# Optimization experiments

Measured on AMD Instinct MI355X. Metric: run time of the kernel, lower is better.

## Reference

```python
import jax, jax.numpy as jnp
import numpy as np
from jax import lax


def unfold(x, k, p, s):
    # torch.nn.functional.unfold: (N,C,H,W) -> (N, C*k*k, L)
    pat = lax.conv_general_dilated_patches(
        x, filter_shape=(k, k), window_strides=(s, s),
        padding=((p, p), (p, p)))
    n, ck2, ho, wo = pat.shape
    return pat.reshape(n, ck2, ho * wo)


def fold(cols, x_shape, k, p, s):
    # torch.nn.functional.fold == adjoint of unfold (overlap-add col2im)
    zero = jnp.zeros(x_shape, cols.dtype)
    _, vjp_fn = jax.vjp(lambda x: unfold(x, k, p, s), zero)
    return vjp_fn(cols)[0]


def setup_inputs() -> dict:
    key = jax.random.key(0)
    ks = jax.random.split(key, 5)
    N, C, H, W = 2, 256, 64, 64
    return {
        "lq_up": jax.random.normal(ks[0], (N, C, H, W), jnp.float32),
        "ref_downup": jax.random.normal(ks[1], (N, C, H, W), jnp.float32),
        "ref0": jax.random.normal(ks[2], (N, C, H, W), jnp.float32),
        "ref1": jax.random.normal(ks[3], (N, C // 2, 2 * H, 2 * W), jnp.float32),
        "ref2": jax.random.normal(ks[4], (N, C // 4, 4 * H, 4 * W), jnp.float32),
    }


def reference(lq_up, ref_downup, ref0, ref1, ref2):
    refs = (ref0, ref1, ref2)
    levels = len(refs)
    n, _, h, w = lq_up.shape

    query = unfold(lq_up, 3, 1, 1)          # (N, C*9, HW)
    key = unfold(ref_downup, 3, 1, 1)       # (N, C*9, HW)
    key_t = jnp.transpose(key, (0, 2, 1))   # (N, HW, C*9)

    eps = 1e-12
    key_t = key_t / jnp.maximum(
        jnp.linalg.norm(key_t, axis=2, keepdims=True), eps)
    query = query / jnp.maximum(
        jnp.linalg.norm(query, axis=1, keepdims=True), eps)

    rel = jnp.matmul(key_t, query)          # (N, HW_k, HW_q)
    max_val = jnp.max(rel, axis=1)          # (N, HW_q)
    max_index = jnp.argmax(rel, axis=1)     # (N, HW_q)

    textures = []
    for i in range(levels):
        k_i, p_i, s_i = 3 * 2 ** i, 2 ** i, 2 ** i
        v = unfold(refs[i], k_i, p_i, s_i)                     # (N, Ci*k*k, HW)
        t = jnp.take_along_axis(v, max_index[:, None, :], axis=2)
        t = fold(t, refs[i].shape, k_i, p_i, s_i) / 9.0
        textures.append(t)

    soft_attention = max_val.reshape(n, 1, h, w)
    return (soft_attention, textures[0], textures[1], textures[2])
```

## Files before the change

### kernel.cpp

```cpp
#include <hip/hip_runtime.h>
#include <math.h>

struct __attribute__((packed)) f4u { float v[4]; };

typedef __attribute__((ext_vector_type(8))) short bf16x8;
typedef __attribute__((ext_vector_type(4))) float f32x4;

#define KCH 16
#define NCH 256
#define LDF 40

__global__ __launch_bounds__(256) void sumsq_k(const float* __restrict__ lq,
                                               const float* __restrict__ refdu,
                                               float* __restrict__ S) {
  const float* src = blockIdx.z ? refdu : lq;
  const int n = blockIdx.y;
  const int h = blockIdx.x * 4 + (threadIdx.x >> 6);
  const int w = threadIdx.x & 63;
  const float* p = src + (size_t)n * 1048576 + h * 64 + w;
  float s0 = 0.f, s1 = 0.f, s2 = 0.f, s3 = 0.f;
  #pragma unroll 4
  for (int c = 0; c < 256; c += 4) {
    float x0 = p[(size_t)c * 4096];
    float x1 = p[(size_t)(c + 1) * 4096];
    float x2 = p[(size_t)(c + 2) * 4096];
    float x3 = p[(size_t)(c + 3) * 4096];
    s0 = fmaf(x0, x0, s0); s1 = fmaf(x1, x1, s1);
    s2 = fmaf(x2, x2, s2); s3 = fmaf(x3, x3, s3);
  }
  S[(blockIdx.z * 2 + n) * 4096 + h * 64 + w] = (s0 + s1) + (s2 + s3);
}

__global__ __launch_bounds__(256) void norm_k(const float* __restrict__ S,
                                              float* __restrict__ qinv,
                                              float* __restrict__ kinv) {
  int idx = blockIdx.x * 256 + threadIdx.x;
  int pix = idx & 4095;
  int nn  = (idx >> 12) & 1;
  int arr = idx >> 13;
  int ph = pix >> 6, pw = pix & 63;
  const float* Sp = S + (arr * 2 + nn) * 4096;
  float sum = 0.f;
  #pragma unroll
  for (int dy = -1; dy <= 1; ++dy) {
    int hh = ph + dy;
    if ((unsigned)hh < 64u) {
      const float* r = Sp + hh * 64;
      #pragma unroll
      for (int dx = -1; dx <= 1; ++dx) {
        int ww = pw + dx;
        if ((unsigned)ww < 64u) sum += r[ww];
      }
    }
  }
  float inv = 1.0f / fmaxf(sqrtf(sum), 1e-12f);
  if (arr) kinv[nn * 4096 + pix] = inv;
  else     qinv[nn * 4096 + pix] = inv;
}

__global__ __launch_bounds__(256) void conv_hl(const float* __restrict__ src,
                                               unsigned short* __restrict__ hi,
                                               unsigned short* __restrict__ lo) {
  int i = (blockIdx.x * 256 + threadIdx.x) * 4;
  float4 v = *reinterpret_cast<const float4*>(src + i);
  ushort4 h, l;
  float xs[4] = {v.x, v.y, v.z, v.w};
  unsigned short hs[4], ls[4];
  #pragma unroll
  for (int j = 0; j < 4; ++j) {
    float x = xs[j];
    unsigned u = __float_as_uint(x);
    unsigned hb = (u + 0x7FFFu + ((u >> 16) & 1u)) & 0xFFFF0000u;
    hs[j] = (unsigned short)(hb >> 16);
    float r = x - __uint_as_float(hb);
    unsigned ur = __float_as_uint(r);
    ls[j] = (unsigned short)((ur + 0x7FFFu + ((ur >> 16) & 1u)) >> 16);
  }
  h = make_ushort4(hs[0], hs[1], hs[2], hs[3]);
  l = make_ushort4(ls[0], ls[1], ls[2], ls[3]);
  *reinterpret_cast<ushort4*>(hi + i) = h;
  *reinterpret_cast<ushort4*>(lo + i) = l;
}

__global__ __launch_bounds__(256) void gemm_mfma(const unsigned short* __restrict__ Ah,
                                                 const unsigned short* __restrict__ Al,
                                                 const unsigned short* __restrict__ Bh,
                                                 const unsigned short* __restrict__ Bl,
                                                 float* __restrict__ Dbase,
                                                 int ldD, int C0, long long dstride) {
  __shared__ unsigned short LAh[64 * LDF], LAl[64 * LDF];
  __shared__ unsigned short LBh[64 * LDF], LBl[64 * LDF];
  const int tid = threadIdx.x;
  const int nz = blockIdx.z;
  const int k0 = blockIdx.x * 64;
  const int dcol0 = blockIdx.y * 64;
  const int jq0 = C0 + dcol0;
  float* D = Dbase + (size_t)nz * dstride;

  const bool oob = (jq0 < 0) || (jq0 + 64 > 4096);

  if (!oob) {
    const unsigned short* Ahb = Ah + (size_t)nz * 1048576;
    const unsigned short* Alb = Al + (size_t)nz * 1048576;
    const unsigned short* Bhb = Bh + (size_t)nz * 1048576;
    const unsigned short* Blb = Bl + (size_t)nz * 1048576;

    const int sh = tid & 1;
    const int mp = (tid >> 1) & 31;
    const int g  = tid >> 6;
    const int rowb = 8 * g + 4 * sh;
    const int colA = k0 + 2 * mp;
    const int colB = jq0 + 2 * mp;
    const int sIdx = (2 * mp) * LDF + g * 8 + sh * 4;

    const int wv = tid >> 6;
    const int lane = tid & 63;
    const int lm = lane & 15;
    const int lg = lane >> 4;
    const int offA = (wv * 16 + lm) * LDF + lg * 8;

    f32x4 acc[4];
    #pragma unroll
    for (int t = 0; t < 4; ++t) acc[t] = (f32x4){0.f, 0.f, 0.f, 0.f};

    for (int ct = 0; ct < 256; ct += 32) {
      __syncthreads();
      {
        const size_t r0 = (size_t)(ct + rowb) * 4096;
        unsigned a0 = *reinterpret_cast<const unsigned*>(Ahb + r0 + colA);
        unsigned a1 = *reinterpret_cast<const unsigned*>(Ahb + r0 + 4096 + colA);
        unsigned a2 = *reinterpret_cast<const unsigned*>(Ahb + r0 + 8192 + colA);
        unsigned a3 = *reinterpret_cast<const unsigned*>(Ahb + r0 + 12288 + colA);
        *reinterpret_cast<ushort4*>(&LAh[sIdx]) =
            make_ushort4(a0 & 0xffff, a1 & 0xffff, a2 & 0xffff, a3 & 0xffff);
        *reinterpret_cast<ushort4*>(&LAh[sIdx + LDF]) =
            make_ushort4(a0 >> 16, a1 >> 16, a2 >> 16, a3 >> 16);
        unsigned c0 = *reinterpret_cast<const unsigned*>(Alb + r0 + colA);
        unsigned c1 = *reinterpret_cast<const unsigned*>(Alb + r0 + 4096 + colA);
        unsigned c2 = *reinterpret_cast<const unsigned*>(Alb + r0 + 8192 + colA);
        unsigned c3 = *reinterpret_cast<const unsigned*>(Alb + r0 + 12288 + colA);
        *reinterpret_cast<ushort4*>(&LAl[sIdx]) =
            make_ushort4(c0 & 0xffff, c1 & 0xffff, c2 & 0xffff, c3 & 0xffff);
        *reinterpret_cast<ushort4*>(&LAl[sIdx + LDF]) =
            make_ushort4(c0 >> 16, c1 >> 16, c2 >> 16, c3 >> 16);
        unsigned b0 = *reinterpret_cast<const unsigned*>(Bhb + r0 + colB);
        unsigned b1 = *reinterpret_cast<const unsigned*>(Bhb + r0 + 4096 + colB);
        unsigned b2 = *reinterpret_cast<const unsigned*>(Bhb + r0 + 8192 + colB);
        unsigned b3 = *reinterpret_cast<const unsigned*>(Bhb + r0 + 12288 + colB);
        *reinterpret_cast<ushort4*>(&LBh[sIdx]) =
            make_ushort4(b0 & 0xffff, b1 & 0xffff, b2 & 0xffff, b3 & 0xffff);
        *reinterpret_cast<ushort4*>(&LBh[sIdx + LDF]) =
            make_ushort4(b0 >> 16, b1 >> 16, b2 >> 16, b3 >> 16);
        unsigned d0 = *reinterpret_cast<const unsigned*>(Blb + r0 + colB);
        unsigned d1 = *reinterpret_cast<const unsigned*>(Blb + r0 + 4096 + colB);
        unsigned d2 = *reinterpret_cast<const unsigned*>(Blb + r0 + 8192 + colB);
        unsigned d3 = *reinterpret_cast<const unsigned*>(Blb + r0 + 12288 + colB);
        *reinterpret_cast<ushort4*>(&LBl[sIdx]) =
            make_ushort4(d0 & 0xffff, d1 & 0xffff, d2 & 0xffff, d3 & 0xffff);
        *reinterpret_cast<ushort4*>(&LBl[sIdx + LDF]) =
            make_ushort4(d0 >> 16, d1 >> 16, d2 >> 16, d3 >> 16);
      }
      __syncthreads();
      bf16x8 a_h = *reinterpret_cast<const bf16x8*>(&LAh[offA]);
      bf16x8 a_l = *reinterpret_cast<const bf16x8*>(&LAl[offA]);
      #pragma unroll
      for (int t = 0; t < 4; ++t) {
        const int offB = (t * 16 + lm) * LDF + lg * 8;
        bf16x8 b_h = *reinterpret_cast<const bf16x8*>(&LBh[offB]);
        bf16x8 b_l = *reinterpret_cast<const bf16x8*>(&LBl[offB]);
        acc[t] = __builtin_amdgcn_mfma_f32_16x16x32_bf16(a_h, b_h, acc[t], 0, 0, 0);
        acc[t] = __builtin_amdgcn_mfma_f32_16x16x32_bf16(a_h, b_l, acc[t], 0, 0, 0);
        acc[t] = __builtin_amdgcn_mfma_f32_16x16x32_bf16(a_l, b_h, acc[t], 0, 0, 0);
      }
    }
    #pragma unroll
    for (int t = 0; t < 4; ++t) {
      #pragma unroll
      for (int r = 0; r < 4; ++r) {
        D[(size_t)(k0 + wv * 16 + lg * 4 + r) * ldD + dcol0 + t * 16 + lm] = acc[t][r];
      }
    }
  } else {
    const int row = tid & 63;
    const int cs = (tid >> 6) * 16;
    float* Dp = D + (size_t)(k0 + row) * ldD + dcol0 + cs;
    #pragma unroll
    for (int j = 0; j < 4; ++j)
      *reinterpret_cast<float4*>(Dp + j * 4) = make_float4(0.f, 0.f, 0.f, 0.f);
  }
}

__global__ __launch_bounds__(256) void reduce_max8(const float* __restrict__ Dbase,
                                                   int ldD, int C0, int Q0,
                                                   const float* __restrict__ kinv,
                                                   float* __restrict__ chunkv,
                                                   int* __restrict__ chunki,
                                                   int n0, long long dstride) {
  __shared__ float sk[KCH];
  const int n = n0 + blockIdx.z;
  const float* D = Dbase + (size_t)blockIdx.z * (size_t)dstride;
  const int k0 = blockIdx.y * KCH;
  const int kh = k0 >> 6;
  const int kwb = k0 & 63;
  if (threadIdx.x < KCH) sk[threadIdx.x] = kinv[n * 4096 + k0 + threadIdx.x];
  __syncthreads();
  const int q0 = Q0 + (blockIdx.x * 256 + threadIdx.x) * 8;
  const int qh = q0 >> 6;
  const int qw0 = q0 & 63;
  const bool up = (kh > 0) && (qh > 0);
  const bool dn = (kh < 63) && (qh < 63);
  const bool lf_ok = qw0 > 0;
  const bool rt_ok = qw0 < 56;
  float best[8]; int bidx[8];
  #pragma unroll
  for (int i = 0; i < 8; ++i) { best[i] = -INFINITY; bidx[i] = k0; }
  const float* Dq = D + (q0 - C0);
  const int step = ldD + 1;
  #pragma unroll 2
  for (int kk = 0; kk < KCH; ++kk) {
    const int kw = kwb + kk;
    const float* P = Dq + (size_t)(k0 + kk) * ldD;
    float r[8];
    {
      float4 c0 = *reinterpret_cast<const float4*>(P);
      float4 c1 = *reinterpret_cast<const float4*>(P + 4);
      r[0]=c0.x; r[1]=c0.y; r[2]=c0.z; r[3]=c0.w; r[4]=c1.x; r[5]=c1.y; r[6]=c1.z; r[7]=c1.w;
    }
    if (up) {
      float4 c0 = *reinterpret_cast<const float4*>(P - 64 * step);
      float4 c1 = *reinterpret_cast<const float4*>(P - 64 * step + 4);
      r[0]+=c0.x; r[1]+=c0.y; r[2]+=c0.z; r[3]+=c0.w; r[4]+=c1.x; r[5]+=c1.y; r[6]+=c1.z; r[7]+=c1.w;
    }
    if (dn) {
      float4 c0 = *reinterpret_cast<const float4*>(P + 64 * step);
      float4 c1 = *reinterpret_cast<const float4*>(P + 64 * step + 4);
      r[0]+=c0.x; r[1]+=c0.y; r[2]+=c0.z; r[3]+=c0.w; r[4]+=c1.x; r[5]+=c1.y; r[6]+=c1.z; r[7]+=c1.w;
    }
    if (kw > 0) {
      #pragma unroll
      for (int t = 0; t < 3; ++t) {
        if (t == 1 && !up) continue;
        if (t == 2 && !dn) continue;
        const int off = (t == 0) ? -step : (t == 1 ? -65 * step : 63 * step);
        f4u b0 = *reinterpret_cast<const f4u*>(P + off);
        f4u b1 = *reinterpret_cast<const f4u*>(P + off + 4);
        r[0] += lf_ok ? b0.v[0] : 0.f; r[1]+=b0.v[1]; r[2]+=b0.v[2]; r[3]+=b0.v[3];
        r[4]+=b1.v[0]; r[5]+=b1.v[1]; r[6]+=b1.v[2]; r[7]+=b1.v[3];
      }
    }
    if (kw < 63) {
      #pragma unroll
      for (int t = 0; t < 3; ++t) {
        if (t == 1 && !up) continue;
        if (t == 2 && !dn) continue;
        const int off = (t == 0) ? step : (t == 1 ? -63 * step : 65 * step);
        f4u b0 = *reinterpret_cast<const f4u*>(P + off);
        f4u b1 = *reinterpret_cast<const f4u*>(P + off + 4);
        r[0]+=b0.v[0]; r[1]+=b0.v[1]; r[2]+=b0.v[2]; r[3]+=b0.v[3];
        r[4]+=b1.v[0]; r[5]+=b1.v[1]; r[6]+=b1.v[2]; r[7] += rt_ok ? b1.v[3] : 0.f;
      }
    }
    const float s = sk[kk];
    const int k = k0 + kk;
    #pragma unroll
    for (int i = 0; i < 8; ++i) {
      float v = r[i] * s;
      if (v > best[i]) { best[i] = v; bidx[i] = k; }
    }
  }
  const int ob = (n * NCH + blockIdx.y) * 4096 + q0;
  *reinterpret_cast<float4*>(chunkv + ob)     = make_float4(best[0], best[1], best[2], best[3]);
  *reinterpret_cast<float4*>(chunkv + ob + 4) = make_float4(best[4], best[5], best[6], best[7]);
  *reinterpret_cast<int4*>(chunki + ob)     = make_int4(bidx[0], bidx[1], bidx[2], bidx[3]);
  *reinterpret_cast<int4*>(chunki + ob + 4) = make_int4(bidx[4], bidx[5], bidx[6], bidx[7]);
}

__global__ __launch_bounds__(256) void combine_k(const float* __restrict__ chunkv,
                                                 const int* __restrict__ chunki,
                                                 const float* __restrict__ qinv,
                                                 float* __restrict__ out_sa,
                                                 int* __restrict__ maxidx, int nch) {
  int t = blockIdx.x * 256 + threadIdx.x;
  int n = t >> 12, q = t & 4095;
  float best = -INFINITY;
  int bi = 0;
  for (int ch = 0; ch < nch; ++ch) {
    int ii = (n * nch + ch) * 4096 + q;
    float v = chunkv[ii];
    int ix = chunki[ii];
    if (v > best) { best = v; bi = ix; }
  }
  maxidx[t] = bi;
  out_sa[t] = best * qinv[t];
}

__global__ __launch_bounds__(256) void gemm_d(const float* __restrict__ Abase,
                                              const float* __restrict__ Bbase,
                                              float* __restrict__ Dbase,
                                              int ldD, int C0, long long dstride) {
  __shared__ __align__(16) float As[2][8][128];
  __shared__ __align__(16) float Bs[2][8][128];
  const int tid = threadIdx.x;
  const int nz = blockIdx.z;
  const int k0 = blockIdx.x * 128;
  const int j0 = blockIdx.y * 128;
  const float* A = Abase + (size_t)nz * 1048576;
  const float* B = Bbase + (size_t)nz * 1048576;
  float* D = Dbase + (size_t)nz * dstride;
  const int ty = tid >> 4, tx = tid & 15, lr = tid >> 5, lc = (tid & 31) << 2;
  float acc[8][8];
  #pragma unroll
  for (int i = 0; i < 8; ++i)
    #pragma unroll
    for (int j = 0; j < 8; ++j) acc[i][j] = 0.f;
  const bool oob = (C0 + j0 < 0) || (C0 + j0 + 128 > 4096);
  if (!oob) {
    const float* Ap = A + k0 + lc;
    const float* Bp = B + (C0 + j0) + lc;
    float4 av = *reinterpret_cast<const float4*>(Ap + (size_t)lr * 4096);
    float4 bv = *reinterpret_cast<const float4*>(Bp + (size_t)lr * 4096);
    *reinterpret_cast<float4*>(&As[0][lr][lc]) = av;
    *reinterpret_cast<float4*>(&Bs[0][lr][lc]) = bv;
    for (int ct = 0; ct < 256; ct += 8) {
      const int buf = (ct >> 3) & 1;
      __syncthreads();
      if (ct + 8 < 256) {
        av = *reinterpret_cast<const float4*>(Ap + (size_t)(ct + 8 + lr) * 4096);
        bv = *reinterpret_cast<const float4*>(Bp + (size_t)(ct + 8 + lr) * 4096);
      }
      #pragma unroll
      for (int kc = 0; kc < 8; ++kc) {
        float a[8], b[8];
        *reinterpret_cast<float4*>(&a[0]) = *reinterpret_cast<const float4*>(&As[buf][kc][ty * 4]);
        *reinterpret_cast<float4*>(&a[4]) = *reinterpret_cast<const float4*>(&As[buf][kc][64 + ty * 4]);
        *reinterpret_cast<float4*>(&b[0]) = *reinterpret_cast<const float4*>(&Bs[buf][kc][tx * 4]);
        *reinterpret_cast<float4*>(&b[4]) = *reinterpret_cast<const float4*>(&Bs[buf][kc][64 + tx * 4]);
        #pragma unroll
        for (int i = 0; i < 8; ++i)
          #pragma unroll
          for (int j = 0; j < 8; ++j)
            acc[i][j] = fmaf(a[i], b[j], acc[i][j]);
      }
      if (ct + 8 < 256) {
        *reinterpret_cast<float4*>(&As[buf ^ 1][lr][lc]) = av;
        *reinterpret_cast<float4*>(&Bs[buf ^ 1][lr][lc]) = bv;
      }
    }
  }
  #pragma unroll
  for (int half = 0; half < 2; ++half)
    #pragma unroll
    for (int i = 0; i < 4; ++i) {
      float* Dp = D + (size_t)(k0 + half * 64 + ty * 4 + i) * ldD + j0;
      *reinterpret_cast<float4*>(Dp + tx * 4)      = *reinterpret_cast<const float4*>(&acc[half * 4 + i][0]);
      *reinterpret_cast<float4*>(Dp + 64 + tx * 4) = *reinterpret_cast<const float4*>(&acc[half * 4 + i][4]);
    }
}

__global__ __launch_bounds__(256) void tex0_lds(const float* __restrict__ ref,
                                                const int* __restrict__ maxidx,
                                                float* __restrict__ outp) {
  __shared__ __align__(16) float4 L[4096];
  const int cq = blockIdx.x;
  const int n  = blockIdx.y;
  const int half = blockIdx.z;
  const int tid = threadIdx.x;
  const float* p0 = ref + (((size_t)n * 256 + cq * 4) << 12);
  for (int i = 0; i < 16; ++i) {
    int px = i * 256 + tid;
    L[px] = make_float4(p0[px], p0[px + 4096], p0[px + 8192], p0[px + 12288]);
  }
  __syncthreads();
  const int* mi = maxidx + n * 4096;
  float* ob = outp + (((size_t)n * 256 + cq * 4) << 12);
  for (int i = 0; i < 8; ++i) {
    int px = half * 2048 + i * 256 + tid;
    int y = px >> 6, x = px & 63;
    float ax = 0.f, ay = 0.f, az = 0.f, aw = 0.f;
    #pragma unroll
    for (int a = -1; a <= 1; ++a) {
      int jh = y + a;
      if ((unsigned)jh < 64u) {
        #pragma unroll
        for (int b = -1; b <= 1; ++b) {
          int jw = x + b;
          if ((unsigned)jw < 64u) {
            int m = mi[jh * 64 + jw];
            int rh = (m >> 6) - a;
            int cx = (m & 63) - b;
            if ((unsigned)rh < 64u && (unsigned)cx < 64u) {
              float4 v = L[rh * 64 + cx];
              ax += v.x; ay += v.y; az += v.z; aw += v.w;
            }
          }
        }
      }
    }
    ob[px]         = ax * (1.f / 9.f);
    ob[px + 4096]  = ay * (1.f / 9.f);
    ob[px + 8192]  = az * (1.f / 9.f);
    ob[px + 12288] = aw * (1.f / 9.f);
  }
}

__global__ __launch_bounds__(256) void tex1_lds(const float* __restrict__ ref,
                                                const int* __restrict__ maxidx,
                                                float* __restrict__ outp) {
  __shared__ __align__(16) float Lf[16384];
  const int c = blockIdx.x;
  const int n = blockIdx.y;
  const int half = blockIdx.z;
  const int tid = threadIdx.x;
  const float* p0 = ref + (((size_t)n * 128 + c) << 14);
  float4* L4 = (float4*)Lf;
  const float4* g4 = (const float4*)p0;
  for (int i = 0; i < 16; ++i) {
    int g = i * 256 + tid;
    L4[g] = g4[g];
  }
  __syncthreads();
  const int* mi = maxidx + n * 4096;
  float* ob = outp + (((size_t)n * 128 + c) << 14);
  for (int i = 0; i < 16; ++i) {
    int pp = half * 4096 + i * 256 + tid;
    int xp = pp & 63;
    int y  = pp >> 6;
    int jh0 = y >> 1;
    float a0 = 0.f, a1 = 0.f;
    #pragma unroll
    for (int a = -1; a <= 1; ++a) {
      int jh = jh0 + a;
      if ((unsigned)jh < 64u) {
        #pragma unroll
        for (int b = -1; b <= 1; ++b) {
          int jw = xp + b;
          if ((unsigned)jw < 64u) {
            int m = mi[jh * 64 + jw];
            int rh = (m >> 6) - a;
            int cx = (m & 63) - b;
            if ((unsigned)rh < 64u && (unsigned)cx < 64u) {
              int off = ((rh << 1) + (y & 1)) * 128 + (cx << 1);
              float2 v = *reinterpret_cast<const float2*>(&Lf[off]);
              a0 += v.x; a1 += v.y;
            }
          }
        }
      }
    }
    *reinterpret_cast<float2*>(&ob[y * 128 + xp * 2]) =
        make_float2(a0 * (1.f / 9.f), a1 * (1.f / 9.f));
  }
}

__global__ __launch_bounds__(256) void tex2_k(const float* __restrict__ ref,
                                              const int* __restrict__ maxidx,
                                              float* __restrict__ outp) {
  int gid = blockIdx.x * 256 + threadIdx.x;
  const int xg = gid & 63;
  const int y  = (gid >> 6) & 255;
  const int cc = (gid >> 14) & 7;
  const int n  = gid >> 17;
  const int jh0 = y >> 2;
  const int* mi = maxidx + n * 4096;
  int offs[9];
  #pragma unroll
  for (int a = -1; a <= 1; ++a) {
    #pragma unroll
    for (int b = -1; b <= 1; ++b) {
      const int t = (a + 1) * 3 + (b + 1);
      int jh = jh0 + a, jw = xg + b;
      int off = -1;
      if ((unsigned)jh < 64u && (unsigned)jw < 64u) {
        int m = mi[jh * 64 + jw];
        int rh = (m >> 6) - jh + jh0;
        int cx = (m & 63) - jw + xg;
        if ((unsigned)rh < 64u && (unsigned)cx < 64u)
          off = ((rh << 2) + (y & 3)) * 256 + (cx << 2);
      }
      offs[t] = off;
    }
  }
  const float* rb = ref + (((size_t)n * 64 + cc * 8) << 16);
  float* ob = outp + ((((size_t)n * 64 + cc * 8) * 256 + y) << 8) + xg * 4;
  #pragma unroll
  for (int i = 0; i < 8; ++i) {
    const float* r = rb + ((size_t)i << 16);
    float4 acc = make_float4(0.f, 0.f, 0.f, 0.f);
    #pragma unroll
    for (int t = 0; t < 9; ++t) {
      if (offs[t] >= 0) {
        float4 v = *reinterpret_cast<const float4*>(r + offs[t]);
        acc.x += v.x; acc.y += v.y; acc.z += v.z; acc.w += v.w;
      }
    }
    acc.x *= (1.f / 9.f); acc.y *= (1.f / 9.f); acc.z *= (1.f / 9.f); acc.w *= (1.f / 9.f);
    *reinterpret_cast<float4*>(ob + ((size_t)i << 16)) = acc;
  }
}

extern "C" void kernel_launch(void* const* d_in, const int* in_sizes, int n_in,
                              void* d_out, int out_size, void* d_ws, size_t ws_size,
                              hipStream_t stream) {
  const float* lq    = (const float*)d_in[0];
  const float* refdu = (const float*)d_in[1];
  const float* ref0  = (const float*)d_in[2];
  const float* ref1  = (const float*)d_in[3];
  const float* ref2  = (const float*)d_in[4];
  float* out = (float*)d_out;

  float* S      = (float*)d_ws;
  float* qinv   = S + 16384;
  float* kinv   = qinv + 8192;
  int*   maxidx = (int*)(kinv + 8192);
  float* chunkv = (float*)(maxidx + 8192);
  int*   chunki = (int*)(chunkv + 2097152);
  unsigned short* Ah = (unsigned short*)(chunki + 2097152);
  unsigned short* Al = Ah + 2097152;
  unsigned short* Bh = Al + 2097152;
  unsigned short* Bl = Bh + 2097152;
  const size_t aux_bytes = (size_t)(40960 + 2097152 + 2097152) * 4 + (size_t)4 * 2097152 * 2;
  float* D = (float*)((char*)d_ws + ((aux_bytes + 255) & ~(size_t)255));

  const int ldD = 4352;
  const size_t Dsz = (size_t)4096 * ldD * 4;
  const long long dstr = (long long)4096 * ldD;
  size_t avail = (ws_size > aux_bytes + 256) ? (ws_size - aux_bytes - 256) : 0;

  sumsq_k<<<dim3(16, 2, 2), 256, 0, stream>>>(lq, refdu, S);
  norm_k<<<dim3(64), 256, 0, stream>>>(S, qinv, kinv);

  if (avail >= 2 * Dsz) {
    conv_hl<<<dim3(2048), 256, 0, stream>>>(refdu, Ah, Al);
    conv_hl<<<dim3(2048), 256, 0, stream>>>(lq, Bh, Bl);
    gemm_mfma<<<dim3(64, 68, 2), 256, 0, stream>>>(Ah, Al, Bh, Bl, D, ldD, -128, dstr);
    reduce_max8<<<dim3(2, NCH, 2), 256, 0, stream>>>(D, ldD, -128, 0, kinv,
                                                     chunkv, chunki, 0, dstr);
  } else if (avail >= Dsz) {
    conv_hl<<<dim3(2048), 256, 0, stream>>>(refdu, Ah, Al);
    conv_hl<<<dim3(2048), 256, 0, stream>>>(lq, Bh, Bl);
    for (int n = 0; n < 2; ++n) {
      gemm_mfma<<<dim3(64, 68, 1), 256, 0, stream>>>(
          Ah + (size_t)n * 1048576, Al + (size_t)n * 1048576,
          Bh + (size_t)n * 1048576, Bl + (size_t)n * 1048576, D, ldD, -128, 0);
      reduce_max8<<<dim3(2, NCH, 1), 256, 0, stream>>>(D, ldD, -128, 0, kinv,
                                                       chunkv, chunki, n, 0);
    }
  } else {
    const int Wq = 2048, ldS = Wq + 256;
    for (int n = 0; n < 2; ++n) {
      for (int Q0 = 0; Q0 < 4096; Q0 += Wq) {
        int C0 = Q0 - 128;
        gemm_d<<<dim3(32, ldS / 128, 1), 256, 0, stream>>>(
            refdu + (size_t)n * 1048576, lq + (size_t)n * 1048576, D, ldS, C0, 0);
        reduce_max8<<<dim3(Wq / 2048, NCH, 1), 256, 0, stream>>>(
            D, ldS, C0, Q0, kinv, chunkv, chunki, n, 0);
      }
    }
  }
  combine_k<<<dim3(32), 256, 0, stream>>>(chunkv, chunki, qinv, out, maxidx, NCH);

  tex0_lds<<<dim3(64, 2, 2),  256, 0, stream>>>(ref0, maxidx, out + 8192);
  tex1_lds<<<dim3(128, 2, 2), 256, 0, stream>>>(ref1, maxidx, out + 2105344);
  tex2_k<<<dim3(1024), 256, 0, stream>>>(ref2, maxidx, out + 6299648);
}
```

Baseline: 434.4 us.

## Transpose bf16 split operands to pixel-major layout for vectorized GEMM tile loads

The hi/lo bf16 conversion kernel now transposes each input from channel-major to pixel-major order, going through a shared-memory tile. This lets the MFMA GEMM load its A and B tiles as contiguous 16-byte vectors per row instead of gathering 4-byte pairs across four channel rows and repacking them. The aim is to cut global load instruction count and the unpacking ALU work in the GEMM inner loop, at the cost of a more complex conversion kernel with LDS transposes and strided shared-memory reads.

```diff
diff --git a/kernel.cpp b/kernel.cpp
--- a/kernel.cpp
+++ b/kernel.cpp
@@ -58,38 +58,56 @@
   else     qinv[nn * 4096 + pix] = inv;
 }
 
-__global__ __launch_bounds__(256) void conv_hl(const float* __restrict__ src,
-                                               unsigned short* __restrict__ hi,
-                                               unsigned short* __restrict__ lo) {
-  int i = (blockIdx.x * 256 + threadIdx.x) * 4;
-  float4 v = *reinterpret_cast<const float4*>(src + i);
-  ushort4 h, l;
-  float xs[4] = {v.x, v.y, v.z, v.w};
-  unsigned short hs[4], ls[4];
+__global__ __launch_bounds__(256) void conv_t(const float* __restrict__ src,
+                                              unsigned short* __restrict__ hi,
+                                              unsigned short* __restrict__ lo) {
+  __shared__ unsigned short Lh[64][68], Ll[64][68];
+  const int tid = threadIdx.x;
+  const int px0 = blockIdx.x * 64;
+  const int c0  = blockIdx.y * 64;
+  const int n   = blockIdx.z;
+  const float* s = src + ((size_t)n * 256 + c0) * 4096 + px0;
+  #pragma unroll
+  for (int i = 0; i < 4; ++i) {
+    int c  = i * 16 + (tid >> 4);
+    int p4 = (tid & 15) * 4;
+    float4 v = *reinterpret_cast<const float4*>(s + (size_t)c * 4096 + p4);
+    float xs[4] = {v.x, v.y, v.z, v.w};
+    #pragma unroll
+    for (int j = 0; j < 4; ++j) {
+      float x = xs[j];
+      unsigned u = __float_as_uint(x);
+      unsigned hb = (u + 0x7FFFu + ((u >> 16) & 1u)) & 0xFFFF0000u;
+      Lh[c][p4 + j] = (unsigned short)(hb >> 16);
+      float r = x - __uint_as_float(hb);
+      unsigned ur = __float_as_uint(r);
+      Ll[c][p4 + j] = (unsigned short)((ur + 0x7FFFu + ((ur >> 16) & 1u)) >> 16);
+    }
+  }
+  __syncthreads();
+  const int px = tid >> 2;
+  const int cq = (tid & 3) * 16;
+  unsigned short hbuf[16], lbuf[16];
+  #pragma unroll
+  for (int j = 0; j < 16; ++j) { hbuf[j] = Lh[cq + j][px]; lbuf[j] = Ll[cq + j][px]; }
+  size_t ob = ((size_t)n * 4096 + px0 + px) * 256 + c0 + cq;
   #pragma unroll
   for (int j = 0; j < 4; ++j) {
-    float x = xs[j];
-    unsigned u = __float_as_uint(x);
-    unsigned hb = (u + 0x7FFFu + ((u >> 16) & 1u)) & 0xFFFF0000u;
-    hs[j] = (unsigned short)(hb >> 16);
-    float r = x - __uint_as_float(hb);
-    unsigned ur = __float_as_uint(r);
-    ls[j] = (unsigned short)((ur + 0x7FFFu + ((ur >> 16) & 1u)) >> 16);
-  }
-  h = make_ushort4(hs[0], hs[1], hs[2], hs[3]);
-  l = make_ushort4(ls[0], ls[1], ls[2], ls[3]);
-  *reinterpret_cast<ushort4*>(hi + i) = h;
-  *reinterpret_cast<ushort4*>(lo + i) = l;
-}
-
-__global__ __launch_bounds__(256) void gemm_mfma(const unsigned short* __restrict__ Ah,
-                                                 const unsigned short* __restrict__ Al,
-                                                 const unsigned short* __restrict__ Bh,
-                                                 const unsigned short* __restrict__ Bl,
+    *reinterpret_cast<ushort4*>(hi + ob + j * 4) =
+        make_ushort4(hbuf[4 * j], hbuf[4 * j + 1], hbuf[4 * j + 2], hbuf[4 * j + 3]);
+    *reinterpret_cast<ushort4*>(lo + ob + j * 4) =
+        make_ushort4(lbuf[4 * j], lbuf[4 * j + 1], lbuf[4 * j + 2], lbuf[4 * j + 3]);
+  }
+}
+
+__global__ __launch_bounds__(256) void gemm_mfma(const unsigned short* __restrict__ At_h,
+                                                 const unsigned short* __restrict__ At_l,
+                                                 const unsigned short* __restrict__ Bt_h,
+                                                 const unsigned short* __restrict__ Bt_l,
                                                  float* __restrict__ Dbase,
                                                  int ldD, int C0, long long dstride) {
-  __shared__ unsigned short LAh[64 * LDF], LAl[64 * LDF];
-  __shared__ unsigned short LBh[64 * LDF], LBl[64 * LDF];
+  __shared__ __align__(16) unsigned short LAh[64 * LDF], LAl[64 * LDF];
+  __shared__ __align__(16) unsigned short LBh[64 * LDF], LBl[64 * LDF];
   const int tid = threadIdx.x;
   const int nz = blockIdx.z;
   const int k0 = blockIdx.x * 64;
@@ -100,18 +118,16 @@
   const bool oob = (jq0 < 0) || (jq0 + 64 > 4096);
 
   if (!oob) {
-    const unsigned short* Ahb = Ah + (size_t)nz * 1048576;
-    const unsigned short* Alb = Al + (size_t)nz * 1048576;
-    const unsigned short* Bhb = Bh + (size_t)nz * 1048576;
-    const unsigned short* Blb = Bl + (size_t)nz * 1048576;
-
-    const int sh = tid & 1;
-    const int mp = (tid >> 1) & 31;
-    const int g  = tid >> 6;
-    const int rowb = 8 * g + 4 * sh;
-    const int colA = k0 + 2 * mp;
-    const int colB = jq0 + 2 * mp;
-    const int sIdx = (2 * mp) * LDF + g * 8 + sh * 4;
+    const unsigned short* Ahb = At_h + (size_t)nz * 1048576;
+    const unsigned short* Alb = At_l + (size_t)nz * 1048576;
+    const unsigned short* Bhb = Bt_h + (size_t)nz * 1048576;
+    const unsigned short* Blb = Bt_l + (size_t)nz * 1048576;
+
+    const int r  = tid >> 2;
+    const int cs = (tid & 3) * 8;
+    const size_t gA = (size_t)(k0 + r) * 256 + cs;
+    const size_t gB = (size_t)(jq0 + r) * 256 + cs;
+    const int sIdx = r * LDF + cs;
 
     const int wv = tid >> 6;
     const int lane = tid & 63;
@@ -126,39 +142,14 @@
     for (int ct = 0; ct < 256; ct += 32) {
       __syncthreads();
       {
-        const size_t r0 = (size_t)(ct + rowb) * 4096;
-        unsigned a0 = *reinterpret_cast<const unsigned*>(Ahb + r0 + colA);
-        unsigned a1 = *reinterpret_cast<const unsigned*>(Ahb + r0 + 4096 + colA);
-        unsigned a2 = *reinterpret_cast<const unsigned*>(Ahb + r0 + 8192 + colA);
-        unsigned a3 = *reinterpret_cast<const unsigned*>(Ahb + r0 + 12288 + colA);
-        *reinterpret_cast<ushort4*>(&LAh[sIdx]) =
-            make_ushort4(a0 & 0xffff, a1 & 0xffff, a2 & 0xffff, a3 & 0xffff);
-        *reinterpret_cast<ushort4*>(&LAh[sIdx + LDF]) =
-            make_ushort4(a0 >> 16, a1 >> 16, a2 >> 16, a3 >> 16);
-        unsigned c0 = *reinterpret_cast<const unsigned*>(Alb + r0 + colA);
-        unsigned c1 = *reinterpret_cast<const unsigned*>(Alb + r0 + 4096 + colA);
-        unsigned c2 = *reinterpret_cast<const unsigned*>(Alb + r0 + 8192 + colA);
-        unsigned c3 = *reinterpret_cast<const unsigned*>(Alb + r0 + 12288 + colA);
-        *reinterpret_cast<ushort4*>(&LAl[sIdx]) =
-            make_ushort4(c0 & 0xffff, c1 & 0xffff, c2 & 0xffff, c3 & 0xffff);
-        *reinterpret_cast<ushort4*>(&LAl[sIdx + LDF]) =
-            make_ushort4(c0 >> 16, c1 >> 16, c2 >> 16, c3 >> 16);
-        unsigned b0 = *reinterpret_cast<const unsigned*>(Bhb + r0 + colB);
-        unsigned b1 = *reinterpret_cast<const unsigned*>(Bhb + r0 + 4096 + colB);
-        unsigned b2 = *reinterpret_cast<const unsigned*>(Bhb + r0 + 8192 + colB);
-        unsigned b3 = *reinterpret_cast<const unsigned*>(Bhb + r0 + 12288 + colB);
-        *reinterpret_cast<ushort4*>(&LBh[sIdx]) =
-            make_ushort4(b0 & 0xffff, b1 & 0xffff, b2 & 0xffff, b3 & 0xffff);
-        *reinterpret_cast<ushort4*>(&LBh[sIdx + LDF]) =
-            make_ushort4(b0 >> 16, b1 >> 16, b2 >> 16, b3 >> 16);
-        unsigned d0 = *reinterpret_cast<const unsigned*>(Blb + r0 + colB);
-        unsigned d1 = *reinterpret_cast<const unsigned*>(Blb + r0 + 4096 + colB);
-        unsigned d2 = *reinterpret_cast<const unsigned*>(Blb + r0 + 8192 + colB);
-        unsigned d3 = *reinterpret_cast<const unsigned*>(Blb + r0 + 12288 + colB);
-        *reinterpret_cast<ushort4*>(&LBl[sIdx]) =
-            make_ushort4(d0 & 0xffff, d1 & 0xffff, d2 & 0xffff, d3 & 0xffff);
-        *reinterpret_cast<ushort4*>(&LBl[sIdx + LDF]) =
-            make_ushort4(d0 >> 16, d1 >> 16, d2 >> 16, d3 >> 16);
+        ulonglong2 vah = *reinterpret_cast<const ulonglong2*>(Ahb + gA + ct);
+        ulonglong2 val = *reinterpret_cast<const ulonglong2*>(Alb + gA + ct);
+        ulonglong2 vbh = *reinterpret_cast<const ulonglong2*>(Bhb + gB + ct);
+        ulonglong2 vbl = *reinterpret_cast<const ulonglong2*>(Blb + gB + ct);
+        *reinterpret_cast<ulonglong2*>(&LAh[sIdx]) = vah;
+        *reinterpret_cast<ulonglong2*>(&LAl[sIdx]) = val;
+        *reinterpret_cast<ulonglong2*>(&LBh[sIdx]) = vbh;
+        *reinterpret_cast<ulonglong2*>(&LBl[sIdx]) = vbl;
       }
       __syncthreads();
       bf16x8 a_h = *reinterpret_cast<const bf16x8*>(&LAh[offA]);
@@ -176,14 +167,14 @@
     #pragma unroll
     for (int t = 0; t < 4; ++t) {
       #pragma unroll
-      for (int r = 0; r < 4; ++r) {
-        D[(size_t)(k0 + wv * 16 + lg * 4 + r) * ldD + dcol0 + t * 16 + lm] = acc[t][r];
+      for (int rr = 0; rr < 4; ++rr) {
+        D[(size_t)(k0 + wv * 16 + lg * 4 + rr) * ldD + dcol0 + t * 16 + lm] = acc[t][rr];
       }
     }
   } else {
     const int row = tid & 63;
-    const int cs = (tid >> 6) * 16;
-    float* Dp = D + (size_t)(k0 + row) * ldD + dcol0 + cs;
+    const int csz = (tid >> 6) * 16;
+    float* Dp = D + (size_t)(k0 + row) * ldD + dcol0 + csz;
     #pragma unroll
     for (int j = 0; j < 4; ++j)
       *reinterpret_cast<float4*>(Dp + j * 4) = make_float4(0.f, 0.f, 0.f, 0.f);
@@ -530,14 +521,14 @@
   norm_k<<<dim3(64), 256, 0, stream>>>(S, qinv, kinv);
 
   if (avail >= 2 * Dsz) {
-    conv_hl<<<dim3(2048), 256, 0, stream>>>(refdu, Ah, Al);
-    conv_hl<<<dim3(2048), 256, 0, stream>>>(lq, Bh, Bl);
+    conv_t<<<dim3(64, 4, 2), 256, 0, stream>>>(refdu, Ah, Al);
+    conv_t<<<dim3(64, 4, 2), 256, 0, stream>>>(lq, Bh, Bl);
     gemm_mfma<<<dim3(64, 68, 2), 256, 0, stream>>>(Ah, Al, Bh, Bl, D, ldD, -128, dstr);
     reduce_max8<<<dim3(2, NCH, 2), 256, 0, stream>>>(D, ldD, -128, 0, kinv,
                                                      chunkv, chunki, 0, dstr);
   } else if (avail >= Dsz) {
-    conv_hl<<<dim3(2048), 256, 0, stream>>>(refdu, Ah, Al);
-    conv_hl<<<dim3(2048), 256, 0, stream>>>(lq, Bh, Bl);
+    conv_t<<<dim3(64, 4, 2), 256, 0, stream>>>(refdu, Ah, Al);
+    conv_t<<<dim3(64, 4, 2), 256, 0, stream>>>(lq, Bh, Bl);
     for (int n = 0; n < 2; ++n) {
       gemm_mfma<<<dim3(64, 68, 1), 256, 0, stream>>>(
           Ah + (size_t)n * 1048576, Al + (size_t)n * 1048576,
```

Measured after the change: 383.7 us (median of 2 runs). 1.13x faster.
